# Kernel tuning notes

Hardware: AMD Instinct MI355X
Metric: run time of the kernel (lower is better)

Reference implementation:

```python
import jax, jax.numpy as jnp
import numpy as np

B, K, S, HS = 32, 8, 512, 256


def setup_inputs() -> dict:
    key = jax.random.key(0)
    ks = jax.random.split(key, 12)
    sc = 1.0 / np.sqrt(HS)
    return {
        "rem_fea": jax.random.normal(ks[0], (B, S, HS), jnp.float32),
        "ret_fea": jax.random.normal(ks[1], (B, K, S, HS), jnp.float32),
        "Wr": jax.random.normal(ks[2], (HS, HS), jnp.float32) * sc,
        "br": jax.random.normal(ks[3], (HS,), jnp.float32) * sc,
        "Wt": jax.random.normal(ks[4], (HS, HS), jnp.float32) * sc,
        "bt": jax.random.normal(ks[5], (HS,), jnp.float32) * sc,
        "W1": jax.random.normal(ks[6], (K, HS, HS), jnp.float32) * sc,
        "b1": jax.random.normal(ks[7], (K, HS), jnp.float32) * sc,
        "W2": jax.random.normal(ks[8], (K, HS, HS), jnp.float32) * sc,
        "b2": jax.random.normal(ks[9], (K, HS), jnp.float32) * sc,
    }


def reference(rem_fea, ret_fea, Wr, br, Wt, bt, W1, b1, W2, b2):
    # ---- MACRouter ----
    rem_lin = rem_fea @ Wr + br                       # [B,S,hs]
    ret_lin = jnp.einsum("bksd,de->bkse", ret_fea, Wt) + bt  # [B,K,S,hs]
    avg_rem = rem_lin.mean(axis=1)                    # [B,hs]
    avg_ret = ret_lin.mean(axis=2)                    # [B,K,hs]
    scores = jnp.einsum("bd,bkd->bk", avg_rem, avg_ret)
    routing = jax.nn.softmax(scores, axis=1)          # [B,K]
    # ---- K dense experts (batched over K) ----
    h = jax.nn.relu(jnp.einsum("bksd,kde->bkse", ret_fea, W1) + b1[None, :, None, :])
    expert_outs = jnp.einsum("bksd,kde->bkse", h, W2) + b2[None, :, None, :]
    # ---- weighted sum over experts ----
    gen_fea = jnp.einsum("bksd,bk->bsd", expert_outs, routing)
    return gen_fea
```

## Files before the change

kernel.cpp:

```cpp
#include <hip/hip_runtime.h>
#include <hip/hip_bf16.h>

typedef __attribute__((ext_vector_type(8))) short bf16x8;
typedef __attribute__((ext_vector_type(4))) float f32x4;

constexpr int Bb = 32, Kk = 8, Ss = 512, HS = 256;
constexpr int MT = 32;
constexpr int NST = Ss / MT;
constexpr int TILE_BYTES = MT * HS * 2;

__device__ __forceinline__ unsigned short f2bf(float f) {
  unsigned int u = __builtin_bit_cast(unsigned int, f);
  u = (u + 0x7FFFu + ((u >> 16) & 1u)) >> 16;
  return (unsigned short)u;
}

__device__ __forceinline__ void gload_lds16(const void* g, void* l) {
  __builtin_amdgcn_global_load_lds((const __attribute__((address_space(1))) void*)g,
                                   (__attribute__((address_space(3))) void*)l, 16, 0, 0);
}

__global__ void prep(const float* __restrict__ rem, const float* __restrict__ ret,
                     const float* __restrict__ W1, const float* __restrict__ W2,
                     unsigned short* __restrict__ W1p, unsigned short* __restrict__ W2p,
                     char* __restrict__ swz, float* __restrict__ partial_ret,
                     float* __restrict__ partial_rem) {
  int blk = blockIdx.x, t = threadIdx.x;
  if (blk < 512) {
    const float* W = (blk < 256) ? W1 : W2;
    unsigned short* Wp = (blk < 256) ? W1p : W2p;
    int idx = (blk & 255) * 256 + t;
    int lane = idx & 63, nt = (idx >> 6) & 15, kk = (idx >> 10) & 7, k = idx >> 13;
    const float* src = W + ((size_t)k * HS + kk * 32 + ((lane >> 4) * 8)) * HS + nt * 16 + (lane & 15);
    unsigned short* dst = Wp + (size_t)idx * 8;
#pragma unroll
    for (int i = 0; i < 8; ++i) dst[i] = f2bf(src[(size_t)i * HS]);
    return;
  }
  blk -= 512;
  const float* src;
  float* pdst;
  char* dst = nullptr;
  if (blk < Bb * Kk * NST) {
    int st = blk & 15, bk = blk >> 4;
    src = ret + ((size_t)bk * Ss + st * MT) * HS;
    pdst = partial_ret + (size_t)blk * HS;
    if (swz) dst = swz + (size_t)blk * TILE_BYTES;
  } else {
    int rid = blk - Bb * Kk * NST;
    int st = rid & 15, b = rid >> 4;
    src = rem + ((size_t)b * Ss + st * MT) * HS;
    pdst = partial_rem + (size_t)rid * HS;
  }
  f32x4 acc = {0.f, 0.f, 0.f, 0.f};
#pragma unroll
  for (int j = 0; j < 8; ++j) {
    int f = j * 256 + t;
    int row = f >> 6, c4 = f & 63;
    f32x4 v = *reinterpret_cast<const f32x4*>(src + (size_t)row * HS + c4 * 4);
    acc += v;
    if (dst) {
      union { unsigned short h[4]; unsigned long long u; } pk;
      pk.h[0] = f2bf(v[0]); pk.h[1] = f2bf(v[1]); pk.h[2] = f2bf(v[2]); pk.h[3] = f2bf(v[3]);
      int off = (c4 >> 5) * 8192 + row * 256 + ((((c4 & 31) >> 1) ^ (row & 7)) * 16) + (c4 & 1) * 8;
      *reinterpret_cast<unsigned long long*>(dst + off) = pk.u;
    }
  }
  __shared__ f32x4 red[256];
  red[t] = acc;
  __syncthreads();
  if (t < 64) {
    f32x4 s = red[t] + red[t + 64] + red[t + 128] + red[t + 192];
    *reinterpret_cast<f32x4*>(pdst + t * 4) = s;
  }
}

__global__ void routing_kernel(const float* __restrict__ partial_ret, const float* __restrict__ partial_rem,
                               const float* __restrict__ Wr, const float* __restrict__ br,
                               const float* __restrict__ Wt, const float* __restrict__ bt,
                               float* __restrict__ routing) {
  int b = blockIdx.x, t = threadIdx.x;
  __shared__ float srem[HS];
  __shared__ float sret[Kk][HS];
  {
    float s = 0.f;
    for (int st = 0; st < NST; ++st) s += partial_rem[((size_t)(b * NST + st)) * HS + t];
    srem[t] = s;
    for (int k = 0; k < Kk; ++k) {
      float sk = 0.f;
      for (int st = 0; st < NST; ++st) sk += partial_ret[((size_t)((b * Kk + k) * NST + st)) * HS + t];
      sret[k][t] = sk;
    }
  }
  __syncthreads();
  float rl = 0.f;
  for (int e = 0; e < HS; ++e) rl += srem[e] * Wr[(size_t)e * HS + t];
  rl = rl * (1.f / Ss) + br[t];
  float tl[Kk];
#pragma unroll
  for (int k = 0; k < Kk; ++k) tl[k] = 0.f;
  for (int e = 0; e < HS; ++e) {
    float w = Wt[(size_t)e * HS + t];
#pragma unroll
    for (int k = 0; k < Kk; ++k) tl[k] += sret[k][e] * w;
  }
  __shared__ float sh[4];
  __shared__ float scores[Kk];
  for (int k = 0; k < Kk; ++k) {
    float p = rl * (tl[k] * (1.f / Ss) + bt[t]);
#pragma unroll
    for (int off = 32; off; off >>= 1) p += __shfl_down(p, off);
    if ((t & 63) == 0) sh[t >> 6] = p;
    __syncthreads();
    if (t == 0) scores[k] = sh[0] + sh[1] + sh[2] + sh[3];
    __syncthreads();
  }
  if (t == 0) {
    float mx = scores[0];
    for (int k = 1; k < Kk; ++k) mx = fmaxf(mx, scores[k]);
    float s = 0.f, ev[Kk];
    for (int k = 0; k < Kk; ++k) { ev[k] = expf(scores[k] - mx); s += ev[k]; }
    for (int k = 0; k < Kk; ++k) routing[b * Kk + k] = ev[k] / s;
  }
}

template <int SRC>
__launch_bounds__(512, 1)
__global__ void experts_kernel(const float* __restrict__ ret, const char* __restrict__ ret_swz,
                               const unsigned short* __restrict__ W1p,
                               const unsigned short* __restrict__ W2p,
                               const float* __restrict__ b1, const float* __restrict__ b2,
                               const float* __restrict__ routing, float* __restrict__ out) {
  __shared__ __align__(16) char A_lds[2][TILE_BYTES];
  __shared__ __align__(16) char H_lds[TILE_BYTES];
  const int blk = blockIdx.x;
  const int b = blk >> 4, st = blk & 15;
  const int tid = threadIdx.x;
  const int wave = tid >> 6, lane = tid & 63;
  const int l15 = lane & 15, l4 = lane >> 4;

  auto stage = [&](int k, int bufi) {
    if constexpr (SRC == 0) {
      const char* tb = ret_swz + ((size_t)((b * Kk + k) * NST + st)) * TILE_BYTES;
#pragma unroll
      for (int i = 0; i < 2; ++i) {
        int c = wave + i * 8;
        gload_lds16(tb + c * 1024 + (size_t)lane * 16, A_lds[bufi] + c * 1024);
      }
    } else {
      const float* src = ret + ((size_t)(b * Kk + k) * Ss + st * MT) * HS;
#pragma unroll
      for (int j = 0; j < 4; ++j) {
        int f = j * 512 + tid;
        int row = f >> 6, c4 = f & 63;
        f32x4 v = *reinterpret_cast<const f32x4*>(src + (size_t)row * HS + c4 * 4);
        union { unsigned short h[4]; unsigned long long u; } pk;
        pk.h[0] = f2bf(v[0]); pk.h[1] = f2bf(v[1]); pk.h[2] = f2bf(v[2]); pk.h[3] = f2bf(v[3]);
        int off = (c4 >> 5) * 8192 + row * 256 + ((((c4 & 31) >> 1) ^ (row & 7)) * 16) + (c4 & 1) * 8;
        *reinterpret_cast<unsigned long long*>(A_lds[bufi] + off) = pk.u;
      }
    }
  };

  float out_acc[2][2][4];
#pragma unroll
  for (int m = 0; m < 2; ++m)
#pragma unroll
    for (int n = 0; n < 2; ++n)
#pragma unroll
      for (int i = 0; i < 4; ++i) out_acc[m][n][i] = 0.f;
  const f32x4 zero4 = {0.f, 0.f, 0.f, 0.f};

  stage(0, 0);
  __syncthreads();

  int buf = 0;
  for (int k = 0; k < Kk; ++k) {
    if (k + 1 < Kk) stage(k + 1, buf ^ 1);

    f32x4 accH[2][2];
#pragma unroll
    for (int m = 0; m < 2; ++m)
#pragma unroll
      for (int n = 0; n < 2; ++n) accH[m][n] = zero4;

    const unsigned short* W1k = W1p + (size_t)k * 65536;
#pragma unroll
    for (int kk = 0; kk < 8; ++kk) {
      bf16x8 aW[2], aA[2];
#pragma unroll
      for (int m = 0; m < 2; ++m)
        aW[m] = *reinterpret_cast<const bf16x8*>(W1k + ((size_t)(kk * 16 + wave * 2 + m) * 64 + lane) * 8);
#pragma unroll
      for (int n = 0; n < 2; ++n) {
        int r = n * 16 + l15;
        int slot = (((kk & 3) * 4 + l4) ^ (r & 7));
        aA[n] = *reinterpret_cast<const bf16x8*>(A_lds[buf] + (kk >> 2) * 8192 + r * 256 + slot * 16);
      }
#pragma unroll
      for (int m = 0; m < 2; ++m)
#pragma unroll
        for (int n = 0; n < 2; ++n)
          accH[m][n] = __builtin_amdgcn_mfma_f32_16x16x32_bf16(aW[m], aA[n], accH[m][n], 0, 0, 0);
    }

#pragma unroll
    for (int m = 0; m < 2; ++m) {
      int e0 = wave * 32 + m * 16 + l4 * 4;
      float4 b1v = *reinterpret_cast<const float4*>(b1 + k * HS + e0);
#pragma unroll
      for (int n = 0; n < 2; ++n) {
        int srow = n * 16 + l15;
        union { unsigned short h[4]; unsigned long long u; } pk;
        pk.h[0] = f2bf(fmaxf(accH[m][n][0] + b1v.x, 0.f));
        pk.h[1] = f2bf(fmaxf(accH[m][n][1] + b1v.y, 0.f));
        pk.h[2] = f2bf(fmaxf(accH[m][n][2] + b1v.z, 0.f));
        pk.h[3] = f2bf(fmaxf(accH[m][n][3] + b1v.w, 0.f));
        int boff = srow * 512 + ((e0 * 2) ^ ((srow & 7) << 4));
        *reinterpret_cast<unsigned long long*>(H_lds + boff) = pk.u;
      }
    }
    __syncthreads();

    f32x4 acc2[2][2];
#pragma unroll
    for (int m = 0; m < 2; ++m)
#pragma unroll
      for (int n = 0; n < 2; ++n) acc2[m][n] = zero4;

    const unsigned short* W2k = W2p + (size_t)k * 65536;
#pragma unroll
    for (int kk = 0; kk < 8; ++kk) {
      bf16x8 aH[2], bW[2];
#pragma unroll
      for (int m = 0; m < 2; ++m) {
        int r = m * 16 + l15;
        int boff = r * 512 + ((kk * 64 + l4 * 16) ^ ((r & 7) << 4));
        aH[m] = *reinterpret_cast<const bf16x8*>(H_lds + boff);
      }
#pragma unroll
      for (int n = 0; n < 2; ++n)
        bW[n] = *reinterpret_cast<const bf16x8*>(W2k + ((size_t)(kk * 16 + wave * 2 + n) * 64 + lane) * 8);
#pragma unroll
      for (int m = 0; m < 2; ++m)
#pragma unroll
        for (int n = 0; n < 2; ++n)
          acc2[m][n] = __builtin_amdgcn_mfma_f32_16x16x32_bf16(aH[m], bW[n], acc2[m][n], 0, 0, 0);
    }

    float rw = routing[b * Kk + k];
#pragma unroll
    for (int n = 0; n < 2; ++n) {
      int col = (wave * 2 + n) * 16 + l15;
      float b2v = b2[k * HS + col];
#pragma unroll
      for (int m = 0; m < 2; ++m)
#pragma unroll
        for (int i = 0; i < 4; ++i) out_acc[m][n][i] += rw * (acc2[m][n][i] + b2v);
    }
    __syncthreads();
    buf ^= 1;
  }

#pragma unroll
  for (int m = 0; m < 2; ++m)
#pragma unroll
    for (int i = 0; i < 4; ++i) {
      int row = m * 16 + l4 * 4 + i;
      float* orow = out + ((size_t)b * Ss + st * MT + row) * HS;
#pragma unroll
      for (int n = 0; n < 2; ++n) orow[(wave * 2 + n) * 16 + l15] = out_acc[m][n][i];
    }
}

extern "C" void kernel_launch(void* const* d_in, const int* in_sizes, int n_in,
                              void* d_out, int out_size, void* d_ws, size_t ws_size,
                              hipStream_t stream) {
  const float* rem = (const float*)d_in[0];
  const float* ret = (const float*)d_in[1];
  const float* Wr  = (const float*)d_in[2];
  const float* br  = (const float*)d_in[3];
  const float* Wt  = (const float*)d_in[4];
  const float* bt  = (const float*)d_in[5];
  const float* W1  = (const float*)d_in[6];
  const float* b1  = (const float*)d_in[7];
  const float* W2  = (const float*)d_in[8];
  const float* b2  = (const float*)d_in[9];
  float* out = (float*)d_out;

  char* w = (char*)d_ws;
  unsigned short* W1p = (unsigned short*)w;
  unsigned short* W2p = (unsigned short*)(w + (1u << 20));
  float* partial_ret  = (float*)(w + (2u << 20));
  float* partial_rem  = (float*)(w + (6u << 20));
  float* routing      = (float*)(w + (6u << 20) + (512u << 10));
  char*  ret_swz      = w + (7u << 20);

  bool full = ws_size >= ((size_t)71 << 20);

  prep<<<512 + Bb * Kk * NST + Bb * NST, 256, 0, stream>>>(rem, ret, W1, W2, W1p, W2p,
                                                           full ? ret_swz : nullptr,
                                                           partial_ret, partial_rem);
  routing_kernel<<<Bb, 256, 0, stream>>>(partial_ret, partial_rem, Wr, br, Wt, bt, routing);
  if (full)
    experts_kernel<0><<<Bb * NST, 512, 0, stream>>>(ret, ret_swz, W1p, W2p, b1, b2, routing, out);
  else
    experts_kernel<1><<<Bb * NST, 512, 0, stream>>>(ret, nullptr, W1p, W2p, b1, b2, routing, out);
}
```

Baseline: 118.5 us.

## Double expert-kernel row tile to 64 and use manual waitcnt barriers

Each expert block now covers 64 sequence rows (two 32-row swizzled sub-tiles) instead of 32, so every W1/W2 fragment loaded from global memory feeds twice as many MFMAs. This halves the grid to 256 blocks and raises per-thread accumulators and LDS use. The two __syncthreads are replaced by inline s_waitcnt plus s_barrier. The risks are fewer blocks than CUs on MI355X (256 CUs), higher register pressure and a longer serial chain per block.

Result: no change. 117.2 us (-1.1%).

```diff
diff --git a/kernel.cpp b/kernel.cpp
--- a/kernel.cpp
+++ b/kernel.cpp
@@ -5,9 +5,10 @@
 typedef __attribute__((ext_vector_type(4))) float f32x4;
 
 constexpr int Bb = 32, Kk = 8, Ss = 512, HS = 256;
-constexpr int MT = 32;
-constexpr int NST = Ss / MT;
-constexpr int TILE_BYTES = MT * HS * 2;
+constexpr int SUB = 32;
+constexpr int NST = Ss / SUB;
+constexpr int SUB_BYTES = SUB * HS * 2;
+constexpr int MT = 64;
 
 __device__ __forceinline__ unsigned short f2bf(float f) {
   unsigned int u = __builtin_bit_cast(unsigned int, f);
@@ -43,13 +44,13 @@
   char* dst = nullptr;
   if (blk < Bb * Kk * NST) {
     int st = blk & 15, bk = blk >> 4;
-    src = ret + ((size_t)bk * Ss + st * MT) * HS;
+    src = ret + ((size_t)bk * Ss + st * SUB) * HS;
     pdst = partial_ret + (size_t)blk * HS;
-    if (swz) dst = swz + (size_t)blk * TILE_BYTES;
+    if (swz) dst = swz + (size_t)blk * SUB_BYTES;
   } else {
     int rid = blk - Bb * Kk * NST;
     int st = rid & 15, b = rid >> 4;
-    src = rem + ((size_t)b * Ss + st * MT) * HS;
+    src = rem + ((size_t)b * Ss + st * SUB) * HS;
     pdst = partial_rem + (size_t)rid * HS;
   }
   f32x4 acc = {0.f, 0.f, 0.f, 0.f};
@@ -131,40 +132,41 @@
                                const unsigned short* __restrict__ W2p,
                                const float* __restrict__ b1, const float* __restrict__ b2,
                                const float* __restrict__ routing, float* __restrict__ out) {
-  __shared__ __align__(16) char A_lds[2][TILE_BYTES];
-  __shared__ __align__(16) char H_lds[TILE_BYTES];
+  __shared__ __align__(16) char A_lds[2][2 * SUB_BYTES];
+  __shared__ __align__(16) char H_lds[MT * HS * 2];
   const int blk = blockIdx.x;
-  const int b = blk >> 4, st = blk & 15;
+  const int b = blk >> 3, st64 = blk & 7;
   const int tid = threadIdx.x;
   const int wave = tid >> 6, lane = tid & 63;
   const int l15 = lane & 15, l4 = lane >> 4;
 
   auto stage = [&](int k, int bufi) {
     if constexpr (SRC == 0) {
-      const char* tb = ret_swz + ((size_t)((b * Kk + k) * NST + st)) * TILE_BYTES;
-#pragma unroll
-      for (int i = 0; i < 2; ++i) {
+      const char* tb = ret_swz + ((size_t)((b * Kk + k) * NST + st64 * 2)) * SUB_BYTES;
+#pragma unroll
+      for (int i = 0; i < 4; ++i) {
         int c = wave + i * 8;
         gload_lds16(tb + c * 1024 + (size_t)lane * 16, A_lds[bufi] + c * 1024);
       }
     } else {
-      const float* src = ret + ((size_t)(b * Kk + k) * Ss + st * MT) * HS;
-#pragma unroll
-      for (int j = 0; j < 4; ++j) {
+      const float* src = ret + ((size_t)(b * Kk + k) * Ss + st64 * MT) * HS;
+#pragma unroll
+      for (int j = 0; j < 8; ++j) {
         int f = j * 512 + tid;
         int row = f >> 6, c4 = f & 63;
         f32x4 v = *reinterpret_cast<const f32x4*>(src + (size_t)row * HS + c4 * 4);
         union { unsigned short h[4]; unsigned long long u; } pk;
         pk.h[0] = f2bf(v[0]); pk.h[1] = f2bf(v[1]); pk.h[2] = f2bf(v[2]); pk.h[3] = f2bf(v[3]);
-        int off = (c4 >> 5) * 8192 + row * 256 + ((((c4 & 31) >> 1) ^ (row & 7)) * 16) + (c4 & 1) * 8;
+        int off = (row >> 5) * 16384 + (c4 >> 5) * 8192 + (row & 31) * 256 +
+                  ((((c4 & 31) >> 1) ^ (row & 7)) * 16) + (c4 & 1) * 8;
         *reinterpret_cast<unsigned long long*>(A_lds[bufi] + off) = pk.u;
       }
     }
   };
 
-  float out_acc[2][2][4];
-#pragma unroll
-  for (int m = 0; m < 2; ++m)
+  float out_acc[4][2][4];
+#pragma unroll
+  for (int m = 0; m < 4; ++m)
 #pragma unroll
     for (int n = 0; n < 2; ++n)
 #pragma unroll
@@ -178,29 +180,31 @@
   for (int k = 0; k < Kk; ++k) {
     if (k + 1 < Kk) stage(k + 1, buf ^ 1);
 
-    f32x4 accH[2][2];
+    f32x4 accH[2][4];
 #pragma unroll
     for (int m = 0; m < 2; ++m)
 #pragma unroll
-      for (int n = 0; n < 2; ++n) accH[m][n] = zero4;
+      for (int n = 0; n < 4; ++n) accH[m][n] = zero4;
 
     const unsigned short* W1k = W1p + (size_t)k * 65536;
 #pragma unroll
     for (int kk = 0; kk < 8; ++kk) {
-      bf16x8 aW[2], aA[2];
+      bf16x8 aW[2], aA[4];
 #pragma unroll
       for (int m = 0; m < 2; ++m)
         aW[m] = *reinterpret_cast<const bf16x8*>(W1k + ((size_t)(kk * 16 + wave * 2 + m) * 64 + lane) * 8);
 #pragma unroll
-      for (int n = 0; n < 2; ++n) {
-        int r = n * 16 + l15;
-        int slot = (((kk & 3) * 4 + l4) ^ (r & 7));
-        aA[n] = *reinterpret_cast<const bf16x8*>(A_lds[buf] + (kk >> 2) * 8192 + r * 256 + slot * 16);
+      for (int n = 0; n < 4; ++n) {
+        int srow = n * 16 + l15;
+        int r5 = srow & 31;
+        int off = (srow >> 5) * 16384 + (kk >> 2) * 8192 + r5 * 256 +
+                  ((((kk & 3) * 4 + l4) ^ (r5 & 7)) * 16);
+        aA[n] = *reinterpret_cast<const bf16x8*>(A_lds[buf] + off);
       }
 #pragma unroll
       for (int m = 0; m < 2; ++m)
 #pragma unroll
-        for (int n = 0; n < 2; ++n)
+        for (int n = 0; n < 4; ++n)
           accH[m][n] = __builtin_amdgcn_mfma_f32_16x16x32_bf16(aW[m], aA[n], accH[m][n], 0, 0, 0);
     }
 
@@ -209,7 +213,7 @@
       int e0 = wave * 32 + m * 16 + l4 * 4;
       float4 b1v = *reinterpret_cast<const float4*>(b1 + k * HS + e0);
 #pragma unroll
-      for (int n = 0; n < 2; ++n) {
+      for (int n = 0; n < 4; ++n) {
         int srow = n * 16 + l15;
         union { unsigned short h[4]; unsigned long long u; } pk;
         pk.h[0] = f2bf(fmaxf(accH[m][n][0] + b1v.x, 0.f));
@@ -220,20 +224,20 @@
         *reinterpret_cast<unsigned long long*>(H_lds + boff) = pk.u;
       }
     }
-    __syncthreads();
-
-    f32x4 acc2[2][2];
-#pragma unroll
-    for (int m = 0; m < 2; ++m)
+    asm volatile("s_waitcnt lgkmcnt(0)\n\ts_barrier" ::: "memory");
+
+    f32x4 acc2[4][2];
+#pragma unroll
+    for (int m = 0; m < 4; ++m)
 #pragma unroll
       for (int n = 0; n < 2; ++n) acc2[m][n] = zero4;
 
     const unsigned short* W2k = W2p + (size_t)k * 65536;
 #pragma unroll
     for (int kk = 0; kk < 8; ++kk) {
-      bf16x8 aH[2], bW[2];
-#pragma unroll
-      for (int m = 0; m < 2; ++m) {
+      bf16x8 aH[4], bW[2];
+#pragma unroll
+      for (int m = 0; m < 4; ++m) {
         int r = m * 16 + l15;
         int boff = r * 512 + ((kk * 64 + l4 * 16) ^ ((r & 7) << 4));
         aH[m] = *reinterpret_cast<const bf16x8*>(H_lds + boff);
@@ -242,7 +246,7 @@
       for (int n = 0; n < 2; ++n)
         bW[n] = *reinterpret_cast<const bf16x8*>(W2k + ((size_t)(kk * 16 + wave * 2 + n) * 64 + lane) * 8);
 #pragma unroll
-      for (int m = 0; m < 2; ++m)
+      for (int m = 0; m < 4; ++m)
 #pragma unroll
         for (int n = 0; n < 2; ++n)
           acc2[m][n] = __builtin_amdgcn_mfma_f32_16x16x32_bf16(aH[m], bW[n], acc2[m][n], 0, 0, 0);
@@ -254,20 +258,20 @@
       int col = (wave * 2 + n) * 16 + l15;
       float b2v = b2[k * HS + col];
 #pragma unroll
-      for (int m = 0; m < 2; ++m)
+      for (int m = 0; m < 4; ++m)
 #pragma unroll
         for (int i = 0; i < 4; ++i) out_acc[m][n][i] += rw * (acc2[m][n][i] + b2v);
     }
-    __syncthreads();
+    asm volatile("s_waitcnt vmcnt(0) lgkmcnt(0)\n\ts_barrier" ::: "memory");
     buf ^= 1;
   }
 
 #pragma unroll
-  for (int m = 0; m < 2; ++m)
+  for (int m = 0; m < 4; ++m)
 #pragma unroll
     for (int i = 0; i < 4; ++i) {
       int row = m * 16 + l4 * 4 + i;
-      float* orow = out + ((size_t)b * Ss + st * MT + row) * HS;
+      float* orow = out + ((size_t)b * Ss + st64 * MT + row) * HS;
 #pragma unroll
       for (int n = 0; n < 2; ++n) orow[(wave * 2 + n) * 16 + l15] = out_acc[m][n][i];
     }
@@ -303,7 +307,7 @@
                                                            partial_ret, partial_rem);
   routing_kernel<<<Bb, 256, 0, stream>>>(partial_ret, partial_rem, Wr, br, Wt, bt, routing);
   if (full)
-    experts_kernel<0><<<Bb * NST, 512, 0, stream>>>(ret, ret_swz, W1p, W2p, b1, b2, routing, out);
+    experts_kernel<0><<<Bb * (Ss / MT), 512, 0, stream>>>(ret, ret_swz, W1p, W2p, b1, b2, routing, out);
   else
-    experts_kernel<1><<<Bb * NST, 512, 0, stream>>>(ret, nullptr, W1p, W2p, b1, b2, routing, out);
-}
+    experts_kernel<1><<<Bb * (Ss / MT), 512, 0, stream>>>(ret, nullptr, W1p, W2p, b1, b2, routing, out);
+}
```
